# Performance work log

Hardware: AMD Instinct MI355X
Metric: run time of the kernel (lower is better)

Reference implementation:

```python
import jax, jax.numpy as jnp
import numpy as np
import math

B, S, HID, H = 2, 1024, 768, 12
D = HID // H  # 64
ALPHA = 32.0


def setup_inputs() -> dict:
    key = jax.random.key(0)
    ks = jax.random.split(key, 8)
    return {
        "hidden_states": jax.random.normal(ks[0], (B, S, HID), jnp.float32),
        "attention_mask": jnp.zeros((B, 1, 1, S), jnp.float32),
        "head_mask": jnp.ones((1, H, 1, 1), jnp.float32),
        "rel_pos": jax.random.normal(ks[1], (B, H, S, S), jnp.float32),
        "rel_2d_pos": jax.random.normal(ks[2], (B, H, S, S), jnp.float32),
        "Wq": jax.random.normal(ks[3], (HID, HID), jnp.float32) * 0.02,
        "bq": jnp.zeros((HID,), jnp.float32),
        "Wk": jax.random.normal(ks[4], (HID, HID), jnp.float32) * 0.02,
        "bk": jnp.zeros((HID,), jnp.float32),
        "Wv": jax.random.normal(ks[5], (HID, HID), jnp.float32) * 0.02,
        "bv": jnp.zeros((HID,), jnp.float32),
    }


def _heads(x):
    # [B,S,HID] -> [B,H,S,D]
    return x.reshape(B, S, H, D).transpose(0, 2, 1, 3)


def cogview_softmax(scores, alpha=ALPHA):
    s = scores / alpha
    m = jnp.max(s, axis=-1, keepdims=True)
    return jax.nn.softmax((s - m) * alpha, axis=-1)


def reference(hidden_states, attention_mask, head_mask, rel_pos, rel_2d_pos,
              Wq, bq, Wk, bk, Wv, bv):
    norm = math.sqrt(D)
    q = _heads(hidden_states @ Wq + bq) / norm   # [B,H,S,D]
    k = _heads(hidden_states @ Wk + bk)
    v = _heads(hidden_states @ Wv + bv)
    scores = jnp.einsum("bhsd,bhtd->bhst", q, k)
    scores = scores + (rel_pos + rel_2d_pos) / norm
    scores = scores + attention_mask
    probs = cogview_softmax(scores)              # [B,H,S,S]
    probs = probs * head_mask
    ctx = jnp.einsum("bhst,bhtd->bhsd", probs, v)
    ctx = ctx.transpose(0, 2, 1, 3).reshape(B, S, HID)
    return ctx
```

## Files before the change

### kernel.cpp

```cpp
#include <hip/hip_runtime.h>
#include <hip/hip_bf16.h>
#include <cstdint>

#define BB   2
#define SS   1024
#define HIDD 768
#define NH   12
#define DH   64
#define BH   (BB*NH)

typedef short bf16x8 __attribute__((ext_vector_type(8)));
typedef float f32x4  __attribute__((ext_vector_type(4)));

__device__ __forceinline__ unsigned short f2b(float x) {
    union { float f; uint32_t u; } v; v.f = x;
    uint32_t u = v.u;
    uint32_t r = (u + 0x7fffu + ((u >> 16) & 1u)) >> 16;
    return (unsigned short)r;
}

__device__ __forceinline__ void async16(const void* g, void* l) {
    __builtin_amdgcn_global_load_lds(
        (const __attribute__((address_space(1))) unsigned int*)g,
        (__attribute__((address_space(3))) unsigned int*)l,
        16, 0, 0);
}

__global__ void cvt_x(const float* __restrict__ x, unsigned short* __restrict__ xb) {
    int i = blockIdx.x * blockDim.x + threadIdx.x;
    float4 v = ((const float4*)x)[i];
    ushort4 o;
    o.x = f2b(v.x); o.y = f2b(v.y); o.z = f2b(v.z); o.w = f2b(v.w);
    ((ushort4*)xb)[i] = o;
}

__global__ void transpose_w(const float* __restrict__ Wq, const float* __restrict__ Wk,
                            const float* __restrict__ Wv, unsigned short* __restrict__ Wt) {
    __shared__ float tile[32][33];
    const int w = blockIdx.z;
    const float* W = (w == 0) ? Wq : (w == 1) ? Wk : Wv;
    const int tx = threadIdx.x & 31, ty = threadIdx.x >> 5;
    const int k0 = blockIdx.x * 32, n0 = blockIdx.y * 32;
    for (int p = 0; p < 4; ++p)
        tile[ty + p * 8][tx] = W[(k0 + ty + p * 8) * HIDD + n0 + tx];
    __syncthreads();
    for (int p = 0; p < 4; ++p) {
        int n = n0 + ty + p * 8;
        Wt[(w * HIDD + n) * HIDD + k0 + tx] = f2b(tile[tx][ty + p * 8]);
    }
}

__global__ __launch_bounds__(256) void qkv_gemm(
    const unsigned short* __restrict__ Xb, const unsigned short* __restrict__ Wt,
    const float* __restrict__ bq, const float* __restrict__ bk, const float* __restrict__ bv,
    unsigned short* __restrict__ Qh, unsigned short* __restrict__ Kh,
    unsigned short* __restrict__ Vh) {
    __shared__ __align__(16) unsigned short lA[2][128 * 32];
    __shared__ __align__(16) unsigned short lB[2][64 * 32];
    const int t = threadIdx.x;
    const int wave = t >> 6, lane = t & 63;
    const int l15 = lane & 15, quad = lane >> 4;
    const int m0 = blockIdx.x * 128;
    const int n0 = blockIdx.y * 64;
    const int wm = wave * 32;

    f32x4 acc[2][4] = {};

    auto stage = [&](int k0, int b) {
        #pragma unroll
        for (int r = 0; r < 2; ++r) {
            int ci = r * 256 + t;
            async16(Xb + (m0 + (ci >> 2)) * HIDD + k0 + (ci & 3) * 8,
                    &lA[b][(r * 256 + wave * 64) * 8]);
        }
        async16(Wt + (n0 + (t >> 2)) * HIDD + k0 + (t & 3) * 8,
                &lB[b][(wave * 64) * 8]);
    };

    stage(0, 0);
    for (int ki = 0; ki < 24; ++ki) {
        const int cur = ki & 1;
        __syncthreads();
        if (ki < 23) stage((ki + 1) * 32, cur ^ 1);
        bf16x8 af[2], bf[4];
        #pragma unroll
        for (int i = 0; i < 2; ++i)
            af[i] = *(const bf16x8*)&lA[cur][(wm + i * 16 + l15) * 32 + quad * 8];
        #pragma unroll
        for (int j = 0; j < 4; ++j)
            bf[j] = *(const bf16x8*)&lB[cur][(j * 16 + l15) * 32 + quad * 8];
        #pragma unroll
        for (int i = 0; i < 2; ++i)
            #pragma unroll
            for (int j = 0; j < 4; ++j)
                acc[i][j] = __builtin_amdgcn_mfma_f32_16x16x32_bf16(af[i], bf[j], acc[i][j], 0, 0, 0);
    }

    const int sect = (n0 >= 1536) ? 2 : (n0 >= 768) ? 1 : 0;
    const float* bias = (sect == 0) ? bq : (sect == 1) ? bk : bv;
    unsigned short* dst = (sect == 0) ? Qh : (sect == 1) ? Kh : Vh;
    const float scale = (sect == 0) ? 0.125f : 1.0f;
    #pragma unroll
    for (int i = 0; i < 2; ++i) {
        #pragma unroll
        for (int j = 0; j < 4; ++j) {
            int n  = n0 + j * 16 + l15;
            int nn = n - sect * HIDD;
            int h = nn >> 6, d = nn & 63;
            float bval = bias[nn];
            #pragma unroll
            for (int r = 0; r < 4; ++r) {
                int m = m0 + wm + i * 16 + quad * 4 + r;
                int b = m >> 10, s = m & 1023;
                float v = (acc[i][j][r] + bval) * scale;
                dst[((size_t)(b * NH + h) * SS + s) * DH + d] = f2b(v);
            }
        }
    }
}

__global__ __launch_bounds__(256) void transpose_v(
    const unsigned short* __restrict__ Vh, unsigned short* __restrict__ VhT) {
    __shared__ unsigned short tile[64][65];
    const int t = threadIdx.x;
    const int bh = blockIdx.y;
    const int s0 = blockIdx.x * 64;
    const int tx = t & 63, ty = t >> 6;
    const unsigned short* src = Vh + (size_t)bh * SS * DH;
    #pragma unroll
    for (int p = 0; p < 16; ++p)
        tile[ty + p * 4][tx] = src[(size_t)(s0 + ty + p * 4) * DH + tx];
    __syncthreads();
    unsigned short* dst = VhT + (size_t)bh * DH * SS;
    #pragma unroll
    for (int p = 0; p < 16; ++p)
        dst[(size_t)(ty + p * 4) * SS + s0 + tx] = tile[tx][ty + p * 4];
}

__global__ __launch_bounds__(128) void flash_attn(
    const unsigned short* __restrict__ Qh, const unsigned short* __restrict__ Kh,
    const unsigned short* __restrict__ VhT,
    const float* __restrict__ rel, const float* __restrict__ rel2d,
    const float* __restrict__ amask, const float* __restrict__ hmask,
    float* __restrict__ out) {
    __shared__ __align__(16) char smemraw[37376];

    const int t = threadIdx.x;
    const int wave = t >> 6, lane = t & 63;
    const int l15 = lane & 15, quad = lane >> 4;
    const int l7 = l15 & 7;
    const int bh = blockIdx.y;
    const int b = bh / NH, h = bh % NH;
    const int m0w = blockIdx.x * 32 + wave * 16;

    const unsigned short* Qp = Qh + (size_t)bh * SS * DH;
    const unsigned short* Kp = Kh + (size_t)bh * SS * DH;
    const unsigned short* Vp = VhT + (size_t)bh * DH * SS;
    const float* relp  = rel   + (size_t)bh * SS * SS;
    const float* rel2p = rel2d + (size_t)bh * SS * SS;
    const float* maskp = amask + (size_t)b * SS;

    unsigned short* Pw = (unsigned short*)(smemraw + 32768) + wave * (16 * 72);

    const float* rowA[4];
    const float* rowB[4];
    #pragma unroll
    for (int r = 0; r < 4; ++r) {
        rowA[r] = relp  + (size_t)(m0w + quad * 4 + r) * SS + l15;
        rowB[r] = rel2p + (size_t)(m0w + quad * 4 + r) * SS + l15;
    }

    auto stage_kv = [&](int j0, int buf) {
        unsigned short* dK = (unsigned short*)(smemraw + buf * 8192);
        unsigned short* dV = (unsigned short*)(smemraw + 16384 + buf * 8192);
        #pragma unroll
        for (int i = 0; i < 4; ++i) {
            int ci = i * 128 + t;
            int row = ci >> 3, sc = ci & 7;
            int g = sc ^ (row & 7);
            async16(Kp + (size_t)(j0 + row) * DH + g * 8,
                    dK + (i * 128 + wave * 64) * 8);
            async16(Vp + (size_t)row * SS + j0 + g * 8,
                    dV + (i * 128 + wave * 64) * 8);
        }
    };

    bf16x8 qf0 = *(const bf16x8*)&Qp[(m0w + l15) * DH + quad * 8];
    bf16x8 qf1 = *(const bf16x8*)&Qp[(m0w + l15) * DH + 32 + quad * 8];

    f32x4 o[4] = {};
    float mrow[4] = {-1e30f, -1e30f, -1e30f, -1e30f};
    float lrow[4] = {0.f, 0.f, 0.f, 0.f};

    float A0[4][4], B0[4][4], A1[4][4], B1[4][4];

    #pragma unroll
    for (int r = 0; r < 4; ++r)
        #pragma unroll
        for (int c = 0; c < 4; ++c) {
            A0[r][c] = rowA[r][c * 16];
            B0[r][c] = rowB[r][c * 16];
        }
    stage_kv(0, 0);
    __syncthreads();

    auto body = [&](int tt, float (&cA)[4][4], float (&cB)[4][4],
                    float (&nA)[4][4], float (&nB)[4][4]) {
        const int j0 = tt * 64, cur = tt & 1;
        const unsigned short* cK = (const unsigned short*)(smemraw + cur * 8192);
        const unsigned short* cV = (const unsigned short*)(smemraw + 16384 + cur * 8192);

        if (tt < 15) {
            #pragma unroll
            for (int r = 0; r < 4; ++r)
                #pragma unroll
                for (int c = 0; c < 4; ++c) {
                    nA[r][c] = rowA[r][j0 + 64 + c * 16];
                    nB[r][c] = rowB[r][j0 + 64 + c * 16];
                }
            stage_kv(j0 + 64, cur ^ 1);
        }

        float mk[4];
        #pragma unroll
        for (int c = 0; c < 4; ++c) mk[c] = maskp[j0 + c * 16 + l15];

        f32x4 sc4[4] = {};
        #pragma unroll
        for (int c = 0; c < 4; ++c) {
            int row = c * 16 + l15;
            bf16x8 k0f = *(const bf16x8*)&cK[row * 64 + (quad ^ l7) * 8];
            bf16x8 k1f = *(const bf16x8*)&cK[row * 64 + ((quad + 4) ^ l7) * 8];
            sc4[c] = __builtin_amdgcn_mfma_f32_16x16x32_bf16(qf0, k0f, sc4[c], 0, 0, 0);
            sc4[c] = __builtin_amdgcn_mfma_f32_16x16x32_bf16(qf1, k1f, sc4[c], 0, 0, 0);
        }

        float sv[4][4];
        #pragma unroll
        for (int c = 0; c < 4; ++c)
            #pragma unroll
            for (int r = 0; r < 4; ++r)
                sv[c][r] = sc4[c][r] + (cA[r][c] + cB[r][c]) * 0.125f + mk[c];

        float alpha[4];
        #pragma unroll
        for (int r = 0; r < 4; ++r) {
            float mx = fmaxf(fmaxf(sv[0][r], sv[1][r]), fmaxf(sv[2][r], sv[3][r]));
            #pragma unroll
            for (int off = 1; off < 16; off <<= 1) mx = fmaxf(mx, __shfl_xor(mx, off, 64));
            float mnew = fmaxf(mrow[r], mx);
            alpha[r] = __expf(mrow[r] - mnew);
            mrow[r] = mnew;
            float rs = 0.f;
            #pragma unroll
            for (int c = 0; c < 4; ++c) {
                float p = __expf(sv[c][r] - mnew);
                sv[c][r] = p;
                rs += p;
            }
            #pragma unroll
            for (int off = 1; off < 16; off <<= 1) rs += __shfl_xor(rs, off, 64);
            lrow[r] = lrow[r] * alpha[r] + rs;
            o[0][r] *= alpha[r]; o[1][r] *= alpha[r]; o[2][r] *= alpha[r]; o[3][r] *= alpha[r];
        }

        #pragma unroll
        for (int c = 0; c < 4; ++c)
            #pragma unroll
            for (int r = 0; r < 4; ++r)
                Pw[(quad * 4 + r) * 72 + c * 16 + l15] = f2b(sv[c][r]);

        bf16x8 pf0 = *(const bf16x8*)&Pw[l15 * 72 + quad * 8];
        bf16x8 pf1 = *(const bf16x8*)&Pw[l15 * 72 + 32 + quad * 8];

        #pragma unroll
        for (int dt = 0; dt < 4; ++dt) {
            int row = dt * 16 + l15;
            bf16x8 v0f = *(const bf16x8*)&cV[row * 64 + (quad ^ l7) * 8];
            bf16x8 v1f = *(const bf16x8*)&cV[row * 64 + ((quad + 4) ^ l7) * 8];
            o[dt] = __builtin_amdgcn_mfma_f32_16x16x32_bf16(pf0, v0f, o[dt], 0, 0, 0);
            o[dt] = __builtin_amdgcn_mfma_f32_16x16x32_bf16(pf1, v1f, o[dt], 0, 0, 0);
        }

        __syncthreads();
    };

    for (int tt = 0; tt < 16; tt += 2) {
        body(tt,     A0, B0, A1, B1);
        body(tt + 1, A1, B1, A0, B0);
    }

    const float hm = hmask[h];
    #pragma unroll
    for (int r = 0; r < 4; ++r) {
        float inv = hm / lrow[r];
        int s = m0w + quad * 4 + r;
        float* op = out + ((size_t)(b * SS + s)) * HIDD + h * DH;
        #pragma unroll
        for (int dt = 0; dt < 4; ++dt) op[dt * 16 + l15] = o[dt][r] * inv;
    }
}

extern "C" void kernel_launch(void* const* d_in, const int* in_sizes, int n_in,
                              void* d_out, int out_size, void* d_ws, size_t ws_size,
                              hipStream_t stream) {
    const float* hs    = (const float*)d_in[0];
    const float* am    = (const float*)d_in[1];
    const float* hm    = (const float*)d_in[2];
    const float* rel   = (const float*)d_in[3];
    const float* rel2d = (const float*)d_in[4];
    const float* Wq    = (const float*)d_in[5];
    const float* bq    = (const float*)d_in[6];
    const float* Wk    = (const float*)d_in[7];
    const float* bk    = (const float*)d_in[8];
    const float* Wv    = (const float*)d_in[9];
    const float* bv    = (const float*)d_in[10];
    float* out = (float*)d_out;

    unsigned short* Xb  = (unsigned short*)d_ws;
    unsigned short* Wt  = Xb + 2048 * HIDD;
    unsigned short* Qh  = Wt + 3 * HIDD * HIDD;
    unsigned short* Kh  = Qh + (size_t)BH * SS * DH;
    unsigned short* Vh  = Kh + (size_t)BH * SS * DH;
    unsigned short* VhT = Vh + (size_t)BH * SS * DH;

    cvt_x<<<(2048 * HIDD / 4) / 256, 256, 0, stream>>>(hs, Xb);
    dim3 gT(24, 24, 3);
    transpose_w<<<gT, 256, 0, stream>>>(Wq, Wk, Wv, Wt);
    dim3 gG(16, 36);
    qkv_gemm<<<gG, 256, 0, stream>>>(Xb, Wt, bq, bk, bv, Qh, Kh, Vh);
    dim3 gV(16, BH);
    transpose_v<<<gV, 256, 0, stream>>>(Vh, VhT);
    dim3 gF(32, BH);
    flash_attn<<<gF, 128, 0, stream>>>(Qh, Kh, VhT, rel, rel2d, am, hm, out);
}
```

Baseline: 278.2 us.

## Triple-buffer K/V and prefetch rel-pos and mask two tiles ahead

The attention loop moves from double to triple buffering of K/V tiles in LDS, and the rel_pos, rel_2d_pos and mask register prefetches now run two tiles ahead instead of one. This is meant to hide more global-memory latency on the bandwidth-heavy bias reads. The full __syncthreads is replaced by a raw s_barrier with a non-blocking vmcnt wait, and s_setprio is raised around the MFMA blocks to favour matrix issue. The extra registers for a third bias set and the larger LDS footprint may lower occupancy. The weaker wait relies on in-order completion of loads to keep cross-wave LDS visibility correct.

```diff
diff --git a/kernel.cpp b/kernel.cpp
--- a/kernel.cpp
+++ b/kernel.cpp
@@ -143,7 +143,7 @@
     const float* __restrict__ rel, const float* __restrict__ rel2d,
     const float* __restrict__ amask, const float* __restrict__ hmask,
     float* __restrict__ out) {
-    __shared__ __align__(16) char smemraw[37376];
+    __shared__ __align__(16) char smemraw[53760];
 
     const int t = threadIdx.x;
     const int wave = t >> 6, lane = t & 63;
@@ -160,19 +160,17 @@
     const float* rel2p = rel2d + (size_t)bh * SS * SS;
     const float* maskp = amask + (size_t)b * SS;
 
-    unsigned short* Pw = (unsigned short*)(smemraw + 32768) + wave * (16 * 72);
+    unsigned short* Pw = (unsigned short*)(smemraw + 49152) + wave * (16 * 72);
 
     const float* rowA[4];
-    const float* rowB[4];
-    #pragma unroll
-    for (int r = 0; r < 4; ++r) {
-        rowA[r] = relp  + (size_t)(m0w + quad * 4 + r) * SS + l15;
-        rowB[r] = rel2p + (size_t)(m0w + quad * 4 + r) * SS + l15;
-    }
+    #pragma unroll
+    for (int r = 0; r < 4; ++r)
+        rowA[r] = relp + (size_t)(m0w + quad * 4 + r) * SS + l15;
+    const size_t d2 = (size_t)(rel2p - relp);
 
     auto stage_kv = [&](int j0, int buf) {
         unsigned short* dK = (unsigned short*)(smemraw + buf * 8192);
-        unsigned short* dV = (unsigned short*)(smemraw + 16384 + buf * 8192);
+        unsigned short* dV = (unsigned short*)(smemraw + 24576 + buf * 8192);
         #pragma unroll
         for (int i = 0; i < 4; ++i) {
             int ci = i * 128 + t;
@@ -192,40 +190,55 @@
     float mrow[4] = {-1e30f, -1e30f, -1e30f, -1e30f};
     float lrow[4] = {0.f, 0.f, 0.f, 0.f};
 
-    float A0[4][4], B0[4][4], A1[4][4], B1[4][4];
-
+    float A0[4][4], B0[4][4], M0[4];
+    float A1[4][4], B1[4][4], M1[4];
+    float A2[4][4], B2[4][4], M2[4];
+
+    stage_kv(0, 0);
+    stage_kv(64, 1);
     #pragma unroll
     for (int r = 0; r < 4; ++r)
         #pragma unroll
         for (int c = 0; c < 4; ++c) {
             A0[r][c] = rowA[r][c * 16];
-            B0[r][c] = rowB[r][c * 16];
-        }
-    stage_kv(0, 0);
-    __syncthreads();
-
-    auto body = [&](int tt, float (&cA)[4][4], float (&cB)[4][4],
-                    float (&nA)[4][4], float (&nB)[4][4]) {
-        const int j0 = tt * 64, cur = tt & 1;
-        const unsigned short* cK = (const unsigned short*)(smemraw + cur * 8192);
-        const unsigned short* cV = (const unsigned short*)(smemraw + 16384 + cur * 8192);
-
-        if (tt < 15) {
+            B0[r][c] = rowA[r][c * 16 + d2];
+        }
+    #pragma unroll
+    for (int c = 0; c < 4; ++c) M0[c] = maskp[c * 16 + l15];
+    #pragma unroll
+    for (int r = 0; r < 4; ++r)
+        #pragma unroll
+        for (int c = 0; c < 4; ++c) {
+            A1[r][c] = rowA[r][64 + c * 16];
+            B1[r][c] = rowA[r][64 + c * 16 + d2];
+        }
+    #pragma unroll
+    for (int c = 0; c < 4; ++c) M1[c] = maskp[64 + c * 16 + l15];
+    asm volatile("s_waitcnt vmcnt(63)" ::: "memory");
+    __builtin_amdgcn_s_barrier();
+
+    auto body = [&](int tt, int bc,
+                    float (&cA)[4][4], float (&cB)[4][4], float (&cM)[4],
+                    float (&nA)[4][4], float (&nB)[4][4], float (&nM)[4]) {
+        const int j0 = tt * 64;
+        const unsigned short* cK = (const unsigned short*)(smemraw + bc * 8192);
+        const unsigned short* cV = (const unsigned short*)(smemraw + 24576 + bc * 8192);
+
+        if (tt <= 13) {
+            stage_kv(j0 + 128, (bc + 2) % 3);
             #pragma unroll
             for (int r = 0; r < 4; ++r)
                 #pragma unroll
                 for (int c = 0; c < 4; ++c) {
-                    nA[r][c] = rowA[r][j0 + 64 + c * 16];
-                    nB[r][c] = rowB[r][j0 + 64 + c * 16];
+                    nA[r][c] = rowA[r][j0 + 128 + c * 16];
+                    nB[r][c] = rowA[r][j0 + 128 + c * 16 + d2];
                 }
-            stage_kv(j0 + 64, cur ^ 1);
-        }
-
-        float mk[4];
-        #pragma unroll
-        for (int c = 0; c < 4; ++c) mk[c] = maskp[j0 + c * 16 + l15];
+            #pragma unroll
+            for (int c = 0; c < 4; ++c) nM[c] = maskp[j0 + 128 + c * 16 + l15];
+        }
 
         f32x4 sc4[4] = {};
+        __builtin_amdgcn_s_setprio(1);
         #pragma unroll
         for (int c = 0; c < 4; ++c) {
             int row = c * 16 + l15;
@@ -234,13 +247,14 @@
             sc4[c] = __builtin_amdgcn_mfma_f32_16x16x32_bf16(qf0, k0f, sc4[c], 0, 0, 0);
             sc4[c] = __builtin_amdgcn_mfma_f32_16x16x32_bf16(qf1, k1f, sc4[c], 0, 0, 0);
         }
+        __builtin_amdgcn_s_setprio(0);
 
         float sv[4][4];
         #pragma unroll
         for (int c = 0; c < 4; ++c)
             #pragma unroll
             for (int r = 0; r < 4; ++r)
-                sv[c][r] = sc4[c][r] + (cA[r][c] + cB[r][c]) * 0.125f + mk[c];
+                sv[c][r] = sc4[c][r] + (cA[r][c] + cB[r][c]) * 0.125f + cM[c];
 
         float alpha[4];
         #pragma unroll
@@ -273,6 +287,7 @@
         bf16x8 pf0 = *(const bf16x8*)&Pw[l15 * 72 + quad * 8];
         bf16x8 pf1 = *(const bf16x8*)&Pw[l15 * 72 + 32 + quad * 8];
 
+        __builtin_amdgcn_s_setprio(1);
         #pragma unroll
         for (int dt = 0; dt < 4; ++dt) {
             int row = dt * 16 + l15;
@@ -281,14 +296,20 @@
             o[dt] = __builtin_amdgcn_mfma_f32_16x16x32_bf16(pf0, v0f, o[dt], 0, 0, 0);
             o[dt] = __builtin_amdgcn_mfma_f32_16x16x32_bf16(pf1, v1f, o[dt], 0, 0, 0);
         }
-
-        __syncthreads();
+        __builtin_amdgcn_s_setprio(0);
+
+        if (tt < 15) {
+            asm volatile("s_waitcnt vmcnt(63)" ::: "memory");
+            __builtin_amdgcn_s_barrier();
+        }
     };
 
-    for (int tt = 0; tt < 16; tt += 2) {
-        body(tt,     A0, B0, A1, B1);
-        body(tt + 1, A1, B1, A0, B0);
-    }
+    for (int tt = 0; tt < 15; tt += 3) {
+        body(tt,     0, A0, B0, M0, A2, B2, M2);
+        body(tt + 1, 1, A1, B1, M1, A0, B0, M0);
+        body(tt + 2, 2, A2, B2, M2, A1, B1, M1);
+    }
+    body(15, 0, A0, B0, M0, A1, B1, M1);
 
     const float hm = hmask[h];
     #pragma unroll
```

Result: no change. 278.7 us (+0.2%).

## Split attention over key chunks and merge partial softmax results in a combine kernel

Applied to the files above, without the earlier changes.

Flash attention is split four ways along the key dimension, giving four times as many blocks. Each block now loads K and V fragments straight from global memory instead of staging them through double-buffered LDS. Partial outputs and running max and sum are written to workspace, and a new combine kernel rescales and merges them, applying the head mask. This is meant to raise parallelism and occupancy, since the kernel is bound by streaming the two large fp32 bias tensors. The cost is an extra launch, extra traffic for the partial results, and loss of the software-pipelined prefetch.

```diff
diff --git a/kernel.cpp b/kernel.cpp
--- a/kernel.cpp
+++ b/kernel.cpp
@@ -8,6 +8,8 @@
 #define NH   12
 #define DH   64
 #define BH   (BB*NH)
+#define KSPLIT 4
+#define KCH  (SS/KSPLIT)
 
 typedef short bf16x8 __attribute__((ext_vector_type(8)));
 typedef float f32x4  __attribute__((ext_vector_type(4)));
@@ -137,53 +139,36 @@
         dst[(size_t)(ty + p * 4) * SS + s0 + tx] = tile[tx][ty + p * 4];
 }
 
-__global__ __launch_bounds__(128) void flash_attn(
+__global__ __launch_bounds__(128, 3) void flash_attn_split(
     const unsigned short* __restrict__ Qh, const unsigned short* __restrict__ Kh,
     const unsigned short* __restrict__ VhT,
     const float* __restrict__ rel, const float* __restrict__ rel2d,
-    const float* __restrict__ amask, const float* __restrict__ hmask,
-    float* __restrict__ out) {
-    __shared__ __align__(16) char smemraw[37376];
+    const float* __restrict__ amask,
+    float* __restrict__ Opart, float* __restrict__ Ml) {
+    __shared__ __align__(16) unsigned short Pbuf[2][16 * 72];
 
     const int t = threadIdx.x;
     const int wave = t >> 6, lane = t & 63;
     const int l15 = lane & 15, quad = lane >> 4;
-    const int l7 = l15 & 7;
     const int bh = blockIdx.y;
-    const int b = bh / NH, h = bh % NH;
+    const int kc = blockIdx.z;
     const int m0w = blockIdx.x * 32 + wave * 16;
+    const int kbase = kc * KCH;
 
     const unsigned short* Qp = Qh + (size_t)bh * SS * DH;
     const unsigned short* Kp = Kh + (size_t)bh * SS * DH;
     const unsigned short* Vp = VhT + (size_t)bh * DH * SS;
     const float* relp  = rel   + (size_t)bh * SS * SS;
     const float* rel2p = rel2d + (size_t)bh * SS * SS;
-    const float* maskp = amask + (size_t)b * SS;
-
-    unsigned short* Pw = (unsigned short*)(smemraw + 32768) + wave * (16 * 72);
+    const float* maskp = amask + (size_t)(bh / NH) * SS;
+
+    unsigned short* Pw = Pbuf[wave];
 
     const float* rowA[4];
-    const float* rowB[4];
-    #pragma unroll
-    for (int r = 0; r < 4; ++r) {
-        rowA[r] = relp  + (size_t)(m0w + quad * 4 + r) * SS + l15;
-        rowB[r] = rel2p + (size_t)(m0w + quad * 4 + r) * SS + l15;
-    }
-
-    auto stage_kv = [&](int j0, int buf) {
-        unsigned short* dK = (unsigned short*)(smemraw + buf * 8192);
-        unsigned short* dV = (unsigned short*)(smemraw + 16384 + buf * 8192);
-        #pragma unroll
-        for (int i = 0; i < 4; ++i) {
-            int ci = i * 128 + t;
-            int row = ci >> 3, sc = ci & 7;
-            int g = sc ^ (row & 7);
-            async16(Kp + (size_t)(j0 + row) * DH + g * 8,
-                    dK + (i * 128 + wave * 64) * 8);
-            async16(Vp + (size_t)row * SS + j0 + g * 8,
-                    dV + (i * 128 + wave * 64) * 8);
-        }
-    };
+    #pragma unroll
+    for (int r = 0; r < 4; ++r)
+        rowA[r] = relp + (size_t)(m0w + quad * 4 + r) * SS + l15;
+    const size_t d2 = (size_t)(rel2p - relp);
 
     bf16x8 qf0 = *(const bf16x8*)&Qp[(m0w + l15) * DH + quad * 8];
     bf16x8 qf1 = *(const bf16x8*)&Qp[(m0w + l15) * DH + 32 + quad * 8];
@@ -192,47 +177,33 @@
     float mrow[4] = {-1e30f, -1e30f, -1e30f, -1e30f};
     float lrow[4] = {0.f, 0.f, 0.f, 0.f};
 
-    float A0[4][4], B0[4][4], A1[4][4], B1[4][4];
-
-    #pragma unroll
-    for (int r = 0; r < 4; ++r)
+    for (int it = 0; it < KSPLIT; ++it) {
+        const int j0 = kbase + it * 64;
+
+        bf16x8 kf0[4], kf1[4];
         #pragma unroll
         for (int c = 0; c < 4; ++c) {
-            A0[r][c] = rowA[r][c * 16];
-            B0[r][c] = rowB[r][c * 16];
-        }
-    stage_kv(0, 0);
-    __syncthreads();
-
-    auto body = [&](int tt, float (&cA)[4][4], float (&cB)[4][4],
-                    float (&nA)[4][4], float (&nB)[4][4]) {
-        const int j0 = tt * 64, cur = tt & 1;
-        const unsigned short* cK = (const unsigned short*)(smemraw + cur * 8192);
-        const unsigned short* cV = (const unsigned short*)(smemraw + 16384 + cur * 8192);
-
-        if (tt < 15) {
-            #pragma unroll
-            for (int r = 0; r < 4; ++r)
-                #pragma unroll
-                for (int c = 0; c < 4; ++c) {
-                    nA[r][c] = rowA[r][j0 + 64 + c * 16];
-                    nB[r][c] = rowB[r][j0 + 64 + c * 16];
-                }
-            stage_kv(j0 + 64, cur ^ 1);
-        }
-
-        float mk[4];
+            const unsigned short* kr = Kp + (size_t)(j0 + c * 16 + l15) * DH;
+            kf0[c] = *(const bf16x8*)&kr[quad * 8];
+            kf1[c] = *(const bf16x8*)&kr[32 + quad * 8];
+        }
+
+        float cA[4][4], cB[4][4], mk[4];
+        #pragma unroll
+        for (int r = 0; r < 4; ++r)
+            #pragma unroll
+            for (int c = 0; c < 4; ++c) {
+                cA[r][c] = rowA[r][j0 + c * 16];
+                cB[r][c] = rowA[r][j0 + c * 16 + d2];
+            }
         #pragma unroll
         for (int c = 0; c < 4; ++c) mk[c] = maskp[j0 + c * 16 + l15];
 
         f32x4 sc4[4] = {};
         #pragma unroll
         for (int c = 0; c < 4; ++c) {
-            int row = c * 16 + l15;
-            bf16x8 k0f = *(const bf16x8*)&cK[row * 64 + (quad ^ l7) * 8];
-            bf16x8 k1f = *(const bf16x8*)&cK[row * 64 + ((quad + 4) ^ l7) * 8];
-            sc4[c] = __builtin_amdgcn_mfma_f32_16x16x32_bf16(qf0, k0f, sc4[c], 0, 0, 0);
-            sc4[c] = __builtin_amdgcn_mfma_f32_16x16x32_bf16(qf1, k1f, sc4[c], 0, 0, 0);
+            sc4[c] = __builtin_amdgcn_mfma_f32_16x16x32_bf16(qf0, kf0[c], sc4[c], 0, 0, 0);
+            sc4[c] = __builtin_amdgcn_mfma_f32_16x16x32_bf16(qf1, kf1[c], sc4[c], 0, 0, 0);
         }
 
         float sv[4][4];
@@ -241,6 +212,14 @@
             #pragma unroll
             for (int r = 0; r < 4; ++r)
                 sv[c][r] = sc4[c][r] + (cA[r][c] + cB[r][c]) * 0.125f + mk[c];
+
+        bf16x8 vf0[4], vf1[4];
+        #pragma unroll
+        for (int dt = 0; dt < 4; ++dt) {
+            const unsigned short* vr = Vp + (size_t)(dt * 16 + l15) * SS + j0;
+            vf0[dt] = *(const bf16x8*)&vr[quad * 8];
+            vf1[dt] = *(const bf16x8*)&vr[32 + quad * 8];
+        }
 
         float alpha[4];
         #pragma unroll
@@ -275,30 +254,54 @@
 
         #pragma unroll
         for (int dt = 0; dt < 4; ++dt) {
-            int row = dt * 16 + l15;
-            bf16x8 v0f = *(const bf16x8*)&cV[row * 64 + (quad ^ l7) * 8];
-            bf16x8 v1f = *(const bf16x8*)&cV[row * 64 + ((quad + 4) ^ l7) * 8];
-            o[dt] = __builtin_amdgcn_mfma_f32_16x16x32_bf16(pf0, v0f, o[dt], 0, 0, 0);
-            o[dt] = __builtin_amdgcn_mfma_f32_16x16x32_bf16(pf1, v1f, o[dt], 0, 0, 0);
-        }
-
-        __syncthreads();
-    };
-
-    for (int tt = 0; tt < 16; tt += 2) {
-        body(tt,     A0, B0, A1, B1);
-        body(tt + 1, A1, B1, A0, B0);
-    }
-
-    const float hm = hmask[h];
-    #pragma unroll
-    for (int r = 0; r < 4; ++r) {
-        float inv = hm / lrow[r];
-        int s = m0w + quad * 4 + r;
-        float* op = out + ((size_t)(b * SS + s)) * HIDD + h * DH;
-        #pragma unroll
-        for (int dt = 0; dt < 4; ++dt) op[dt * 16 + l15] = o[dt][r] * inv;
-    }
+            o[dt] = __builtin_amdgcn_mfma_f32_16x16x32_bf16(pf0, vf0[dt], o[dt], 0, 0, 0);
+            o[dt] = __builtin_amdgcn_mfma_f32_16x16x32_bf16(pf1, vf1[dt], o[dt], 0, 0, 0);
+        }
+    }
+
+    float* Op = Opart + ((size_t)(kc * BH + bh) * SS + m0w) * DH;
+    #pragma unroll
+    for (int r = 0; r < 4; ++r)
+        #pragma unroll
+        for (int dt = 0; dt < 4; ++dt)
+            Op[(quad * 4 + r) * DH + dt * 16 + l15] = o[dt][r];
+    if (l15 == 0) {
+        #pragma unroll
+        for (int r = 0; r < 4; ++r) {
+            size_t row = (size_t)(kc * BH + bh) * SS + m0w + quad * 4 + r;
+            Ml[row * 2]     = mrow[r];
+            Ml[row * 2 + 1] = lrow[r];
+        }
+    }
+}
+
+__global__ __launch_bounds__(256) void combine(
+    const float* __restrict__ Opart, const float* __restrict__ Ml,
+    const float* __restrict__ hmask, float* __restrict__ out) {
+    const int gid = blockIdx.x * 256 + threadIdx.x;
+    const int d  = gid & 63;
+    const int s  = (gid >> 6) & (SS - 1);
+    const int bh = gid >> 16;
+    const int b = bh / NH, h = bh % NH;
+    const size_t CH = (size_t)BH * SS * DH;
+    const size_t row = (size_t)bh * SS + s;
+    const size_t RML = (size_t)BH * SS;
+
+    float m[KSPLIT], l[KSPLIT];
+    #pragma unroll
+    for (int kc = 0; kc < KSPLIT; ++kc) {
+        m[kc] = Ml[(kc * RML + row) * 2];
+        l[kc] = Ml[(kc * RML + row) * 2 + 1];
+    }
+    float M = fmaxf(fmaxf(m[0], m[1]), fmaxf(m[2], m[3]));
+    float num = 0.f, den = 0.f;
+    #pragma unroll
+    for (int kc = 0; kc < KSPLIT; ++kc) {
+        float w = __expf(m[kc] - M);
+        num += Opart[kc * CH + row * DH + d] * w;
+        den += l[kc] * w;
+    }
+    out[((size_t)b * SS + s) * HIDD + h * DH + d] = hmask[h] * num / den;
 }
 
 extern "C" void kernel_launch(void* const* d_in, const int* in_sizes, int n_in,
@@ -323,6 +326,8 @@
     unsigned short* Kh  = Qh + (size_t)BH * SS * DH;
     unsigned short* Vh  = Kh + (size_t)BH * SS * DH;
     unsigned short* VhT = Vh + (size_t)BH * SS * DH;
+    float* Opart = (float*)(VhT + (size_t)BH * SS * DH);
+    float* Ml    = Opart + (size_t)KSPLIT * BH * SS * DH;
 
     cvt_x<<<(2048 * HIDD / 4) / 256, 256, 0, stream>>>(hs, Xb);
     dim3 gT(24, 24, 3);
@@ -331,6 +336,7 @@
     qkv_gemm<<<gG, 256, 0, stream>>>(Xb, Wt, bq, bk, bv, Qh, Kh, Vh);
     dim3 gV(16, BH);
     transpose_v<<<gV, 256, 0, stream>>>(Vh, VhT);
-    dim3 gF(32, BH);
-    flash_attn<<<gF, 128, 0, stream>>>(Qh, Kh, VhT, rel, rel2d, am, hm, out);
-}
+    dim3 gF(32, BH, KSPLIT);
+    flash_attn_split<<<gF, 128, 0, stream>>>(Qh, Kh, VhT, rel, rel2d, am, Opart, Ml);
+    combine<<<(BH * SS * DH) / 256, 256, 0, stream>>>(Opart, Ml, hm, out);
+}
```

After: 310.1 us. 11.5% more time.
